# Optimization experiments

Measured on AMD Instinct MI355X. Metric: run time of the kernel, lower is better.

The kernel has to match this reference:

```python
import jax, jax.numpy as jnp
import numpy as np

B, L, D = 32, 512, 128          # batch, seq_len, d_model (= num graph nodes N)
E, HS, DTR, U = 64, 64, 4, 32   # d_proj_E, d_proj_H (state), dt_rank, d_proj_U
R, K, DE, NH = 3, 3, 10, 4      # mamba layers, cheb order, d_e, heads
EPS = 1e-5


def _ln(x, g, b):
    m = jnp.mean(x, -1, keepdims=True)
    v = jnp.mean((x - m) ** 2, -1, keepdims=True)
    return (x - m) / jnp.sqrt(v + EPS) * g + b


def _mamba(x, in_w, conv_w, conv_b, xproj_w, dt_w, dt_b, Alog, Dp, out_w):
    b, l, _ = x.shape
    xz = x @ in_w                                  # (b,l,2E)
    xp, res = xz[..., :E], xz[..., E:]
    xc = jnp.transpose(xp, (0, 2, 1))              # (b,E,l)
    # causal depthwise conv: torch pads both sides by d_conv-1 then slices [:l]
    xc = jax.lax.conv_general_dilated(
        xc, conv_w, (1,), [(conv_w.shape[-1] - 1, 0)],
        dimension_numbers=('NCH', 'OIH', 'NCH'), feature_group_count=E)
    xc = xc + conv_b[None, :, None]
    xp = jax.nn.silu(jnp.transpose(xc, (0, 2, 1)))  # (b,l,E)
    xdbl = xp @ xproj_w                             # (b,l,DTR+2*HS)
    delta = jax.nn.softplus(xdbl[..., :DTR] @ dt_w + dt_b)        # (b,l,E)
    Bm = xdbl[..., DTR:DTR + HS]                                   # (b,l,HS)
    Cm = xdbl[..., DTR + HS:]                                      # (b,l,HS)
    A = -jnp.exp(Alog)                                             # (E,HS)
    dA = jnp.exp(delta[..., None] * A)                             # (b,l,E,HS)
    dBu = delta[..., None] * Bm[:, :, None, :] * xp[..., None]     # (b,l,E,HS)

    def step(s, t):
        dA_t, dBu_t, C_t = t
        s = dA_t * s + dBu_t
        return s, jnp.einsum('bdn,bn->bd', s, C_t)

    _, ys = jax.lax.scan(step, jnp.zeros((b, E, HS), x.dtype),
                         (jnp.swapaxes(dA, 0, 1), jnp.swapaxes(dBu, 0, 1),
                          jnp.swapaxes(Cm, 0, 1)))
    y = jnp.swapaxes(ys, 0, 1) + xp * Dp
    y = y * jax.nn.sigmoid(res)
    return y @ out_w


def _forward(x, mb_in_w, mb_conv_w, mb_conv_b, mb_xproj_w, mb_dt_w, mb_dt_b,
             mb_Alog, mb_D, mb_out_w, ln1_g, ln1_b, ln2_g, ln2_b,
             ffn_w1, ffn_b1, ffn_w2, ffn_b2,
             psi_emb, psi, W_q, W_k, attn_alpha, F_w, f_b, head_mix,
             head_w, head_b):
    # ---- bidirectional Mamba stack ----
    for i in range(R):
        f, bk = 2 * i, 2 * i + 1
        Y1 = _mamba(x, mb_in_w[f], mb_conv_w[f], mb_conv_b[f], mb_xproj_w[f],
                    mb_dt_w[f], mb_dt_b[f], mb_Alog[f], mb_D[f], mb_out_w[f])
        Y2 = jnp.flip(_mamba(jnp.flip(x, 1), mb_in_w[bk], mb_conv_w[bk],
                             mb_conv_b[bk], mb_xproj_w[bk], mb_dt_w[bk],
                             mb_dt_b[bk], mb_Alog[bk], mb_D[bk], mb_out_w[bk]), 1)
        Y3 = _ln(x + Y1 + Y2, ln1_g[i], ln1_b[i])
        Yp = jax.nn.relu(Y3 @ ffn_w1[i] + ffn_b1[i]) @ ffn_w2[i] + ffn_b2[i]
        x = _ln(Yp + Y3, ln2_g[i], ln2_b[i])
    h = jnp.transpose(x, (0, 2, 1))                # (B, N=D, L)
    # ---- MAGAC (deterministic single MC sample, eval, no edge drop) ----
    diff = psi_emb[:, None, :] - psi_emb[None, :, :]
    A_g = jax.nn.softmax(jnp.exp(-psi * jnp.sum(diff * diff, -1)), axis=1)
    Q = jnp.einsum('nd,dhm->nhm', psi_emb, W_q)
    Kt = jnp.einsum('nd,dhm->nhm', psi_emb, W_k)
    attn = jax.nn.softmax(jnp.einsum('nhd,mhd->hnm', Q, Kt)
                          / jnp.sqrt(jnp.asarray(DE, x.dtype)), axis=-1)
    alpha = jax.nn.sigmoid(attn_alpha)
    A_effs = alpha * A_g[None] + (1.0 - alpha) * attn   # (H,N,N)
    mix = jax.nn.softmax(head_mix)
    I = jnp.eye(D, dtype=x.dtype)
    out = jnp.zeros((x.shape[0], D), x.dtype)
    for hh in range(NH):
        A = A_effs[hh]
        sup = [I, A]
        for _ in range(2, K + 1):
            sup.append(2.0 * A @ sup[-1] - sup[-2])
        S = jnp.stack(sup, 0)                             # (K+1,N,N)
        Wf = jnp.einsum('nd,dkl->nkl', psi_emb, F_w[hh])  # (N,K+1,L)
        bf = psi_emb @ f_b[hh]                            # (N,)
        out_h = jnp.einsum('knm,bml,nkl->bn', S, h, Wf) + bf
        out = out + mix[hh] * out_h
    log_var = jnp.zeros_like(out)
    pred = out @ head_w + head_b                          # (B,1)
    return pred, log_var


def setup_inputs() -> dict:
    key = jax.random.key(0)
    ks = iter(jax.random.split(key, 40))
    nrm = lambda shp, s=0.05: (jax.random.normal(next(ks), shp, jnp.float32) * s)
    M = 2 * R
    base_Alog = jnp.log(jnp.arange(1, HS + 1, dtype=jnp.float32))
    inp = {
        'x': jax.random.normal(next(ks), (B, L, D), jnp.float32),
        'mb_in_w': nrm((M, D, 2 * E)),
        'mb_conv_w': nrm((M, E, 1, 3), 0.2),
        'mb_conv_b': jnp.zeros((M, E), jnp.float32),
        'mb_xproj_w': nrm((M, E, DTR + 2 * HS)),
        'mb_dt_w': nrm((M, DTR, E), 0.2),
        'mb_dt_b': jnp.zeros((M, E), jnp.float32),
        'mb_Alog': jnp.tile(base_Alog[None, None, :], (M, E, 1)),
        'mb_D': jnp.ones((M, E), jnp.float32),
        'mb_out_w': nrm((M, E, D)),
        'ln1_g': jnp.ones((R, D), jnp.float32),
        'ln1_b': jnp.zeros((R, D), jnp.float32),
        'ln2_g': jnp.ones((R, D), jnp.float32),
        'ln2_b': jnp.zeros((R, D), jnp.float32),
        'ffn_w1': nrm((R, D, U)),
        'ffn_b1': jnp.zeros((R, U), jnp.float32),
        'ffn_w2': nrm((R, U, D)),
        'ffn_b2': jnp.zeros((R, D), jnp.float32),
        'psi_emb': jax.random.normal(next(ks), (D, DE), jnp.float32),
        'psi': jnp.asarray(1.0, jnp.float32),
        'W_q': jax.random.normal(next(ks), (DE, NH, DE), jnp.float32),
        'W_k': jax.random.normal(next(ks), (DE, NH, DE), jnp.float32),
        'attn_alpha': jnp.asarray(0.5, jnp.float32),
        'F_w': nrm((NH, DE, K + 1, L), 0.05),
        'f_b': nrm((NH, DE), 1.0),
        'head_mix': jnp.ones((NH,), jnp.float32),
        'head_w': nrm((D, 1)),
        'head_b': jnp.zeros((1,), jnp.float32),
    }
    return inp


def reference(x, mb_in_w, mb_conv_w, mb_conv_b, mb_xproj_w, mb_dt_w, mb_dt_b,
              mb_Alog, mb_D, mb_out_w, ln1_g, ln1_b, ln2_g, ln2_b,
              ffn_w1, ffn_b1, ffn_w2, ffn_b2,
              psi_emb, psi, W_q, W_k, attn_alpha, F_w, f_b, head_mix,
              head_w, head_b):
    return _forward(x, mb_in_w, mb_conv_w, mb_conv_b, mb_xproj_w, mb_dt_w,
                    mb_dt_b, mb_Alog, mb_D, mb_out_w, ln1_g, ln1_b, ln2_g,
                    ln2_b, ffn_w1, ffn_b1, ffn_w2, ffn_b2, psi_emb, psi,
                    W_q, W_k, attn_alpha, F_w, f_b, head_mix, head_w, head_b)
```

## Files before the change

### kernel.cpp

```cpp
#include <hip/hip_runtime.h>
#include <hip/hip_bf16.h>


#define B_ 32
#define L_ 512
#define D_ 128
#define E_ 64
#define HS_ 64

#define OFF_X     0u
#define OFF_XZF   2097152u
#define OFF_XZB   4194304u
#define OFF_XPF   6291456u
#define OFF_XPB   7340032u
#define OFF_PKF   8388608u
#define OFF_PKB   10485760u
#define OFF_XBCF  12582912u
#define OFF_XBCB  14680064u
#define OFF_YSF   16777216u
#define OFF_YSB   17825792u
#define OFF_V     2097152u
#define OFF_WFT   10485760u
#define OFF_STT   11534336u
#define OFF_AEFF  11796480u
#define OFF_QB    11943936u
#define OFF_KB    11949056u
#define OFF_MIX   11954176u
#define OFF_ALPH  11954180u
#define OFF_BFT   11954184u
#define OFF_PART  12582912u
#define OFF_RED1  16777216u

__device__ __forceinline__ float sigf(float x) { return 1.f / (1.f + __expf(-x)); }
__device__ __forceinline__ unsigned int bf16r(float x) {
    unsigned int u = __float_as_uint(x);
    return (u + 0x7fffu + ((u >> 16) & 1u)) >> 16;
}

__global__ __launch_bounds__(256) void gemm_in2_kernel(
    const float* __restrict__ X, const float* __restrict__ WF, const float* __restrict__ WB,
    float* __restrict__ xzF, float* __restrict__ xzB)
{
    __shared__ float sxT[128][36];
    __shared__ float sw[2][16][128];
    const int tid = threadIdx.x;
    const int r0 = blockIdx.x * 32;
    for (int q = tid; q < 1024; q += 256) {
        const int r = q >> 5, k4 = q & 31;
        const float4 v = *(const float4*)&X[(size_t)(r0 + r) * 128 + k4 * 4];
        sxT[k4 * 4 + 0][r] = v.x; sxT[k4 * 4 + 1][r] = v.y;
        sxT[k4 * 4 + 2][r] = v.z; sxT[k4 * 4 + 3][r] = v.w;
    }
    const int wv = tid >> 6, lane = tid & 63;
    const int d = wv >> 1, ch = wv & 1;
    const int r4 = lane >> 4, c16 = lane & 15;
    float4 acc[8];
#pragma unroll
    for (int j = 0; j < 8; ++j) acc[j] = float4{0.f, 0.f, 0.f, 0.f};
    for (int ko = 0; ko < 128; ko += 16) {
        __syncthreads();
        for (int q = tid; q < 1024; q += 256) {
            const int dd = q >> 9, kk = (q >> 5) & 15, c4 = q & 31;
            *(float4*)&sw[dd][kk][c4 * 4] =
                *(const float4*)&((dd ? WB : WF)[(ko + kk) * 128 + c4 * 4]);
        }
        __syncthreads();
#pragma unroll
        for (int kk = 0; kk < 16; ++kk) {
            const float4 w4 = *(const float4*)&sw[d][kk][ch * 64 + c16 * 4];
            const float4 xa = *(const float4*)&sxT[ko + kk][r4 * 8];
            const float4 xb = *(const float4*)&sxT[ko + kk][r4 * 8 + 4];
            const float xs[8] = {xa.x, xa.y, xa.z, xa.w, xb.x, xb.y, xb.z, xb.w};
#pragma unroll
            for (int j = 0; j < 8; ++j) {
                acc[j].x = fmaf(xs[j], w4.x, acc[j].x);
                acc[j].y = fmaf(xs[j], w4.y, acc[j].y);
                acc[j].z = fmaf(xs[j], w4.z, acc[j].z);
                acc[j].w = fmaf(xs[j], w4.w, acc[j].w);
            }
        }
    }
    float* xz = d ? xzB : xzF;
#pragma unroll
    for (int j = 0; j < 8; ++j) {
        *(float4*)&xz[(r0 + r4 * 8 + j) * 128 + ch * 64 + c16 * 4] = acc[j];
    }
}

__global__ __launch_bounds__(256) void prep4_kernel(
    const float* __restrict__ xzF_, const float* __restrict__ xzB_,
    const float* __restrict__ conv_w, const float* __restrict__ conv_b,
    const float* __restrict__ xproj_w, const float* __restrict__ dt_w,
    const float* __restrict__ dt_b, int layer,
    float* __restrict__ xpF_, float* __restrict__ xpB_,
    unsigned int* __restrict__ xbcF_, unsigned int* __restrict__ xbcB_,
    float* __restrict__ pkF_, float* __restrict__ pkB_)
{
    __shared__ float sW[8448];
    __shared__ float sxp4[4][64][4];
    __shared__ float sdl4[4][4][4];
    const int tid = threadIdx.x, wv = tid >> 6, lane = tid & 63;
    const int dir = (int)(blockIdx.x >= 1024);
    const int r0 = (blockIdx.x & 1023) * 16;
    const int b = r0 >> 9;
    const int m = layer * 2 + dir;
    const float* Wg = xproj_w + m * 8448;
    for (int q = tid; q < 2112; q += 256) ((float4*)sW)[q] = ((const float4*)Wg)[q];
    const float* xz = dir ? xzB_ : xzF_;
    float* xp  = dir ? xpB_  : xpF_;
    unsigned int* xbc = dir ? xbcB_ : xbcF_;
    float* pkx = dir ? pkB_  : pkF_;
    const float* cw = conv_w + m * 192 + lane * 3;
    const float cw0 = cw[0], cw1 = cw[1], cw2 = cw[2];
    const float cb  = conv_b[m * 64 + lane];
    const float dtb = dt_b[m * 64 + lane];
    const float* dwp = dt_w + m * 256;
    const float dw0 = dwp[lane], dw1 = dwp[64 + lane], dw2 = dwp[128 + lane], dw3 = dwp[192 + lane];
    float uu[4];
#pragma unroll
    for (int it = 0; it < 4; ++it) {
        const int row = r0 + wv * 4 + it;
        const int l = row & 511;
        const int l1 = dir ? l + 1 : l - 1;
        const int l2 = dir ? l + 2 : l - 2;
        float acc = cb;
        const float x0 = xz[(size_t)row * 128 + lane];
        const float x1 = (l1 >= 0 && l1 < 512) ? xz[(size_t)(b * 512 + l1) * 128 + lane] : 0.f;
        const float x2 = (l2 >= 0 && l2 < 512) ? xz[(size_t)(b * 512 + l2) * 128 + lane] : 0.f;
        acc += cw0 * x2 + cw1 * x1 + cw2 * x0;
        const float u = acc * sigf(acc);
        xp[row * 64 + lane] = u;
        uu[it] = u;
    }
    *(float4*)&sxp4[wv][lane][0] = float4{uu[0], uu[1], uu[2], uu[3]};
    __syncthreads();
    const int jdt = lane & 3;
    float aB[4] = {0.f, 0.f, 0.f, 0.f};
    float aC[4] = {0.f, 0.f, 0.f, 0.f};
    float adt[4] = {0.f, 0.f, 0.f, 0.f};
#pragma unroll 4
    for (int k = 0; k < 64; ++k) {
        const float wB = sW[k * 132 + 4 + lane];
        const float wC = sW[k * 132 + 68 + lane];
        const float wd = sW[k * 132 + jdt];
        const float4 xv = *(const float4*)&sxp4[wv][k][0];
        aB[0] = fmaf(xv.x, wB, aB[0]); aC[0] = fmaf(xv.x, wC, aC[0]); adt[0] = fmaf(xv.x, wd, adt[0]);
        aB[1] = fmaf(xv.y, wB, aB[1]); aC[1] = fmaf(xv.y, wC, aC[1]); adt[1] = fmaf(xv.y, wd, adt[1]);
        aB[2] = fmaf(xv.z, wB, aB[2]); aC[2] = fmaf(xv.z, wC, aC[2]); adt[2] = fmaf(xv.z, wd, adt[2]);
        aB[3] = fmaf(xv.w, wB, aB[3]); aC[3] = fmaf(xv.w, wC, aC[3]); adt[3] = fmaf(xv.w, wd, adt[3]);
    }
#pragma unroll
    for (int it = 0; it < 4; ++it) {
        const int row = r0 + wv * 4 + it;
        xbc[row * 64 + lane] = (bf16r(aC[it]) << 16) | bf16r(aB[it]);
        if (lane < 4) sdl4[wv][it][lane] = adt[it];
    }
#pragma unroll
    for (int it = 0; it < 4; ++it) {
        const int row = r0 + wv * 4 + it;
        float dpre = fmaf(sdl4[wv][it][0], dw0, dtb);
        dpre = fmaf(sdl4[wv][it][1], dw1, dpre);
        dpre = fmaf(sdl4[wv][it][2], dw2, dpre);
        dpre = fmaf(sdl4[wv][it][3], dw3, dpre);
        const float dlt = (dpre > 20.f) ? dpre : log1pf(__expf(dpre));
        ((float2*)pkx)[row * 64 + lane] = float2{dlt, dlt * uu[it]};
    }
}

__global__ __launch_bounds__(256, 4) void scan7_kernel(
    const unsigned int* __restrict__ xbcF, const unsigned int* __restrict__ xbcB,
    const float* __restrict__ pkF, const float* __restrict__ pkB,
    const float* __restrict__ AlogF, const float* __restrict__ AlogB,
    float* __restrict__ ysF, float* __restrict__ ysB)
{
    __shared__ unsigned int sbc[2][1024];
    __shared__ float spk[2][4][16][2];
    __shared__ float ytile[4][16][68];
    const int tid = threadIdx.x, wv = tid >> 6, lane = tid & 63;
    const int bx = blockIdx.x;
    const int db = bx & 63;
    const int dir = db >> 5;
    const int b   = db & 31;
    const int e0  = (bx >> 6) * 4;
    const int e   = e0 + wv;
    const unsigned int* xbc = dir ? xbcB : xbcF;
    const float* pk  = dir ? pkB  : pkF;
    const float* Aw  = dir ? AlogB : AlogF;
    float* ys = dir ? ysB : ysF;
    const float a = -__expf(Aw[e * 64 + lane]);
    float s = 0.f;
    float* yrow = ys + (size_t)(b * 64 + e) * 512;

    const int psl = tid & 15, pw_ = tid >> 4;

#define STG_LOAD(RS)                                                              \
    {                                                                             \
        nb = *(const uint4*)(xbc + (size_t)(RS) * 64 + tid * 4);                  \
        if (tid < 64)                                                             \
            npp = *(const float2*)(pk + (size_t)((RS) + psl) * 128 + (e0 + pw_) * 2); \
    }
#define STG_WRITE(BUF)                                                            \
    {                                                                             \
        *(uint4*)(&sbc[BUF][tid * 4]) = nb;                                       \
        if (tid < 64) *(float2*)(&spk[BUF][pw_][psl][0]) = npp;                   \
    }

#define SCAN16(REV)                                                               \
    {                                                                             \
        const unsigned int* bc = &sbc[cur][0];                                    \
        const float* pq = &spk[cur][wv][0][0];                                    \
        _Pragma("unroll")                                                         \
        for (int j = 0; j < 8; ++j) {                                             \
            const int pj = (REV) ? 7 - j : j;                                     \
            const float4 pk4 = *(const float4*)(pq + pj * 4);                     \
            const int sA = (REV) ? 15 - 2 * j : 2 * j;                            \
            const int sB = (REV) ? 14 - 2 * j : 2 * j + 1;                        \
            const float dlA = (REV) ? pk4.z : pk4.x;                              \
            const float duA = (REV) ? pk4.w : pk4.y;                              \
            const float dlB = (REV) ? pk4.x : pk4.z;                              \
            const float duB = (REV) ? pk4.y : pk4.w;                              \
            const unsigned int bA = bc[sA * 64 + lane];                           \
            const float BnA = __uint_as_float(bA << 16);                          \
            const float CnA = __uint_as_float(bA & 0xffff0000u);                  \
            s = fmaf(__expf(dlA * a), s, duA * BnA);                              \
            ytile[wv][2 * j][lane] = s * CnA;                                     \
            const unsigned int bB = bc[sB * 64 + lane];                           \
            const float BnB = __uint_as_float(bB << 16);                          \
            const float CnB = __uint_as_float(bB & 0xffff0000u);                  \
            s = fmaf(__expf(dlB * a), s, duB * BnB);                              \
            ytile[wv][2 * j + 1][lane] = s * CnB;                                 \
        }                                                                         \
    }

    {
        uint4 nb; float2 npp;
        const int rs0 = b * 512 + (dir ? 496 : 0);
        STG_LOAD(rs0);
        STG_WRITE(0);
    }
    __syncthreads();

    int cur = 0;
    const int rr = lane & 15, sg = lane >> 4;
    for (int t = 0; t < 32; ++t) {
        uint4 nb; float2 npp;
        const bool more = (t + 1) < 32;
        if (more) {
            const int rs = b * 512 + (dir ? (496 - (t + 1) * 16) : ((t + 1) * 16));
            STG_LOAD(rs);
        }
        if (dir == 0) { SCAN16(0) } else { SCAN16(1) }
        {
            const float* yt = &ytile[wv][rr][sg * 16];
            const float4 A0 = *(const float4*)yt;
            const float4 A1 = *(const float4*)(yt + 4);
            const float4 A2 = *(const float4*)(yt + 8);
            const float4 A3 = *(const float4*)(yt + 12);
            float p = ((A0.x + A0.y) + (A0.z + A0.w)) + ((A1.x + A1.y) + (A1.z + A1.w))
                    + ((A2.x + A2.y) + (A2.z + A2.w)) + ((A3.x + A3.y) + (A3.z + A3.w));
            p += __shfl_xor(p, 16);
            p += __shfl_xor(p, 32);
            if (lane < 16) {
                const int lg = dir ? (511 - (t * 16 + rr)) : (t * 16 + rr);
                yrow[lg] = p;
            }
        }
        if (more) STG_WRITE(cur ^ 1);
        __syncthreads();
        cur ^= 1;
    }
#undef STG_LOAD
#undef STG_WRITE
#undef SCAN16
}

__global__ __launch_bounds__(256) void opfn_kernel(
    const float* __restrict__ ysF, const float* __restrict__ ysB,
    const float* __restrict__ xpF, const float* __restrict__ xpB,
    const float* __restrict__ xzF, const float* __restrict__ xzB,
    const float* __restrict__ Dp, int layer,
    const float* __restrict__ Xc, const float* __restrict__ out_w,
    const float* __restrict__ W1, const float* __restrict__ b1,
    const float* __restrict__ W2, const float* __restrict__ b2,
    const float* __restrict__ g1, const float* __restrict__ bb1,
    const float* __restrict__ g2, const float* __restrict__ bb2,
    float* __restrict__ xout)
{
    __shared__ float smem[8832];
    float* syt = smem;
    float* y3  = smem;
    float* sy  = smem + 2176;
    float* sw  = smem + 4224;
    float* sh  = smem + 8320;
    const int tid = threadIdx.x;
    const int r0 = blockIdx.x * 16;
    const int b = r0 >> 9, l0 = r0 & 511;

    for (int q = tid; q < 512; q += 256) {
        const int d = q >> 8, ee = (q >> 2) & 63, rq = q & 3;
        const float* ysp = d ? ysB : ysF;
        const float4 v = *(const float4*)&ysp[(size_t)(b * 64 + ee) * 512 + l0 + rq * 4];
        float* dst = &syt[(d * 64 + ee) * 17 + rq * 4];
        dst[0] = v.x; dst[1] = v.y; dst[2] = v.z; dst[3] = v.w;
    }
    __syncthreads();
    for (int q = tid; q < 2048; q += 256) {
        const int r = q >> 7, c = q & 127;
        const int d = c >> 6, ee = c & 63;
        const int row = r0 + r;
        const float dv  = Dp[(layer * 2 + d) * 64 + ee];
        const float u   = (d ? xpB : xpF)[(size_t)row * 64 + ee];
        const float res = (d ? xzB : xzF)[(size_t)row * 128 + 64 + ee];
        sy[r * 128 + c] = (syt[(d * 64 + ee) * 17 + r] + u * dv) * sigf(res);
    }
    const int wv = tid >> 6, lane = tid & 63;
    const float* WFp = out_w + (layer * 2) * 8192;
    const float* WBp = out_w + (layer * 2 + 1) * 8192;
    float acc[4][2];
#pragma unroll
    for (int r = 0; r < 4; ++r) { acc[r][0] = 0.f; acc[r][1] = 0.f; }
    for (int ko = 0; ko < 128; ko += 32) {
        __syncthreads();
        for (int q = tid; q < 1024; q += 256) {
            const int kk = q >> 5, c4 = q & 31;
            const int kg = ko + kk;
            *(float4*)&sw[kk * 128 + c4 * 4] = (kg < 64)
                ? *(const float4*)&WFp[kg * 128 + c4 * 4]
                : *(const float4*)&WBp[(kg - 64) * 128 + c4 * 4];
        }
        __syncthreads();
#define OPSTEP(COMP, J)                                                           \
        {                                                                         \
            const float w0 = sw[(kk + (J)) * 128 + lane];                         \
            const float w1 = sw[(kk + (J)) * 128 + lane + 64];                    \
            acc[0][0] = fmaf(y40.COMP, w0, acc[0][0]);                            \
            acc[0][1] = fmaf(y40.COMP, w1, acc[0][1]);                            \
            acc[1][0] = fmaf(y41.COMP, w0, acc[1][0]);                            \
            acc[1][1] = fmaf(y41.COMP, w1, acc[1][1]);                            \
            acc[2][0] = fmaf(y42.COMP, w0, acc[2][0]);                            \
            acc[2][1] = fmaf(y42.COMP, w1, acc[2][1]);                            \
            acc[3][0] = fmaf(y43.COMP, w0, acc[3][0]);                            \
            acc[3][1] = fmaf(y43.COMP, w1, acc[3][1]);                            \
        }
#pragma unroll
        for (int kk = 0; kk < 32; kk += 4) {
            const float4 y40 = *(const float4*)&sy[(wv * 4 + 0) * 128 + ko + kk];
            const float4 y41 = *(const float4*)&sy[(wv * 4 + 1) * 128 + ko + kk];
            const float4 y42 = *(const float4*)&sy[(wv * 4 + 2) * 128 + ko + kk];
            const float4 y43 = *(const float4*)&sy[(wv * 4 + 3) * 128 + ko + kk];
            OPSTEP(x, 0) OPSTEP(y, 1) OPSTEP(z, 2) OPSTEP(w, 3)
        }
#undef OPSTEP
    }
    __syncthreads();
    for (int q = tid; q < 1024; q += 256) ((float4*)sw)[q] = ((const float4*)W1)[q];
#pragma unroll
    for (int r = 0; r < 4; ++r) {
        const int rl = wv * 4 + r;
        const int row = r0 + rl;
        float v0 = acc[r][0] + Xc[(size_t)row * 128 + lane];
        float v1 = acc[r][1] + Xc[(size_t)row * 128 + lane + 64];
        float sum = v0 + v1, sq = v0 * v0 + v1 * v1;
#pragma unroll
        for (int o = 32; o >= 1; o >>= 1) { sum += __shfl_xor(sum, o); sq += __shfl_xor(sq, o); }
        const float mean = sum * (1.f / 128.f);
        const float var = sq * (1.f / 128.f) - mean * mean;
        const float rs = rsqrtf(var + 1e-5f);
        y3[rl * 128 + lane]      = (v0 - mean) * rs * g1[lane] + bb1[lane];
        y3[rl * 128 + lane + 64] = (v1 - mean) * rs * g1[lane + 64] + bb1[lane + 64];
    }
    __syncthreads();
    {
        const int r = tid >> 4, u = tid & 15;
        float h0 = b1[u], h1 = b1[u + 16];
#pragma unroll 8
        for (int k = 0; k < 128; ++k) {
            const float xv = y3[r * 128 + k];
            h0 = fmaf(xv, sw[k * 32 + u], h0);
            h1 = fmaf(xv, sw[k * 32 + u + 16], h1);
        }
        sh[r * 32 + u]      = fmaxf(h0, 0.f);
        sh[r * 32 + u + 16] = fmaxf(h1, 0.f);
    }
    __syncthreads();
    for (int q = tid; q < 1024; q += 256) ((float4*)sw)[q] = ((const float4*)W2)[q];
    __syncthreads();
#pragma unroll
    for (int r = 0; r < 4; ++r) {
        const int rl = wv * 4 + r;
        float a0 = b2[lane], a1 = b2[lane + 64];
#pragma unroll 8
        for (int k = 0; k < 32; ++k) {
            const float hv = sh[rl * 32 + k];
            a0 = fmaf(hv, sw[k * 128 + lane], a0);
            a1 = fmaf(hv, sw[k * 128 + lane + 64], a1);
        }
        const float v0 = a0 + y3[rl * 128 + lane];
        const float v1 = a1 + y3[rl * 128 + lane + 64];
        float sum = v0 + v1, sq = v0 * v0 + v1 * v1;
#pragma unroll
        for (int o = 32; o >= 1; o >>= 1) { sum += __shfl_xor(sum, o); sq += __shfl_xor(sq, o); }
        const float mean = sum * (1.f / 128.f);
        const float var = sq * (1.f / 128.f) - mean * mean;
        const float rs = rsqrtf(var + 1e-5f);
        const int row = r0 + rl;
        xout[(size_t)row * 128 + lane]      = (v0 - mean) * rs * g2[lane] + bb2[lane];
        xout[(size_t)row * 128 + lane + 64] = (v1 - mean) * rs * g2[lane + 64] + bb2[lane + 64];
    }
}

__global__ __launch_bounds__(256) void head_prep_kernel(
    const float* __restrict__ psi, const float* __restrict__ W_q, const float* __restrict__ W_k,
    const float* __restrict__ f_b, const float* __restrict__ hmix, const float* __restrict__ attn_a,
    float* __restrict__ mixb, float* __restrict__ alphab, float* __restrict__ bft,
    float* __restrict__ Qb, float* __restrict__ Kb)
{
    const int tid = threadIdx.x;
    const float m0 = hmix[0], m1 = hmix[1], m2 = hmix[2], m3 = hmix[3];
    const float mx = fmaxf(fmaxf(m0, m1), fmaxf(m2, m3));
    const float e0 = __expf(m0 - mx), e1 = __expf(m1 - mx), e2 = __expf(m2 - mx), e3 = __expf(m3 - mx);
    const float inv = 1.f / (e0 + e1 + e2 + e3);
    float mixv[4] = {e0 * inv, e1 * inv, e2 * inv, e3 * inv};
    if (tid < 4) mixb[tid] = mixv[tid];
    if (tid == 4) alphab[0] = sigf(attn_a[0]);
    if (tid < 128) {
        float s = 0.f;
        for (int h = 0; h < 4; ++h) {
            float t = 0.f;
            for (int d = 0; d < 10; ++d) t = fmaf(psi[tid * 10 + d], f_b[h * 10 + d], t);
            s = fmaf(mixv[h], t, s);
        }
        bft[tid] = s;
    }
    for (int idx = tid; idx < 5120; idx += 256) {
        const int n = idx / 40, rem = idx - n * 40, h = rem / 10, d = rem - h * 10;
        float q = 0.f, kk = 0.f;
        for (int d0 = 0; d0 < 10; ++d0) {
            const float pv = psi[n * 10 + d0];
            q = fmaf(pv, W_q[(d0 * 4 + h) * 10 + d], q);
            kk = fmaf(pv, W_k[(d0 * 4 + h) * 10 + d], kk);
        }
        Qb[idx] = q; Kb[idx] = kk;
    }
}

__global__ __launch_bounds__(128) void head_qkaeff_kernel(
    const float* __restrict__ psi, const float* __restrict__ psis,
    const float* __restrict__ Qb, const float* __restrict__ Kb,
    const float* __restrict__ alphab,
    float* __restrict__ Aeff, float* __restrict__ StT)
{
    __shared__ float spn[10];
    __shared__ float red[128];
    const int h = blockIdx.x >> 7, n = blockIdx.x & 127, mcol = threadIdx.x;
    if (mcol < 10) spn[mcol] = psi[n * 10 + mcol];
    __syncthreads();
    float d2 = 0.f;
#pragma unroll
    for (int d = 0; d < 10; ++d) { const float df = spn[d] - psi[mcol * 10 + d]; d2 = fmaf(df, df, d2); }
    const float gv = __expf(-psis[0] * d2);
    float qv = 0.f;
#pragma unroll
    for (int d = 0; d < 10; ++d) qv = fmaf(Qb[n * 40 + h * 10 + d], Kb[mcol * 40 + h * 10 + d], qv);
    qv *= 0.3162277660168379332f;
    float r;
    red[mcol] = gv; __syncthreads();
    for (int s = 64; s >= 1; s >>= 1) { if (mcol < s) red[mcol] = fmaxf(red[mcol], red[mcol + s]); __syncthreads(); }
    r = red[0]; __syncthreads();
    const float eg = __expf(gv - r);
    red[mcol] = eg; __syncthreads();
    for (int s = 64; s >= 1; s >>= 1) { if (mcol < s) red[mcol] += red[mcol + s]; __syncthreads(); }
    const float gsum = red[0]; __syncthreads();
    red[mcol] = qv; __syncthreads();
    for (int s = 64; s >= 1; s >>= 1) { if (mcol < s) red[mcol] = fmaxf(red[mcol], red[mcol + s]); __syncthreads(); }
    r = red[0]; __syncthreads();
    const float eq = __expf(qv - r);
    red[mcol] = eq; __syncthreads();
    for (int s = 64; s >= 1; s >>= 1) { if (mcol < s) red[mcol] += red[mcol + s]; __syncthreads(); }
    const float qsum = red[0];
    const float al = alphab[0];
    const float aeff = al * (eg / gsum) + (1.f - al) * (eq / qsum);
    Aeff[h * 16384 + n * 128 + mcol] = aeff;
    StT[((h * 4 + 1) * 128 + mcol) * 128 + n] = aeff;
    StT[((h * 4 + 0) * 128 + mcol) * 128 + n] = (mcol == n) ? 1.f : 0.f;
}

__global__ __launch_bounds__(256) void head_cheb_kernel(
    const float* __restrict__ Aeff, float* __restrict__ StT, int kk)
{
    const int h = blockIdx.x >> 6;
    const int m0 = ((blockIdx.x & 63) << 1) + (threadIdx.x >> 7);
    const int n = threadIdx.x & 127;
    const float* Ar = Aeff + h * 16384 + n * 128;
    const float* Sp = StT + ((h * 4 + kk - 1) * 128 + m0) * 128;
    float acc = 0.f;
#pragma unroll 8
    for (int p = 0; p < 128; ++p) acc = fmaf(Ar[p], Sp[p], acc);
    const float s2 = StT[((h * 4 + kk - 2) * 128 + m0) * 128 + n];
    StT[((h * 4 + kk) * 128 + m0) * 128 + n] = 2.f * acc - s2;
}

__global__ __launch_bounds__(256) void head_wf_kernel(
    const float* __restrict__ psi, const float* __restrict__ F_w, float* __restrict__ WfT)
{
    const int idx = blockIdx.x * 256 + threadIdx.x;
    const int n = idx & 127, l = (idx >> 7) & 511, k = (idx >> 16) & 3, h = idx >> 18;
    float acc = 0.f;
#pragma unroll
    for (int d = 0; d < 10; ++d)
        acc = fmaf(psi[n * 10 + d], F_w[((h * 10 + d) * 4 + k) * 512 + l], acc);
    WfT[idx] = acc;
}

__global__ __launch_bounds__(256) void head_v4_kernel(
    const float* __restrict__ StT, const float* __restrict__ WfT, const float* __restrict__ mixb,
    float* __restrict__ V)
{
    const int tid = threadIdx.x;
    const int lt = blockIdx.x & 63, mm = blockIdx.x >> 6;
    const int n4 = tid & 31, mh = tid >> 5;
    const int m = mm * 8 + mh;
    const int l0 = lt * 8, n0 = n4 * 4;
    float4 sv[16];
#pragma unroll
    for (int h = 0; h < 4; ++h) {
        const float mx = mixb[h];
#pragma unroll
        for (int k = 0; k < 4; ++k) {
            const float4 v = *(const float4*)&StT[(size_t)((h * 4 + k) * 128 + m) * 128 + n0];
            sv[h * 4 + k] = float4{v.x * mx, v.y * mx, v.z * mx, v.w * mx};
        }
    }
#pragma unroll
    for (int j = 0; j < 8; ++j) {
        const int l = l0 + j;
        float4 acc = {0.f, 0.f, 0.f, 0.f};
#pragma unroll
        for (int hk = 0; hk < 16; ++hk) {
            const float4 w = *(const float4*)&WfT[(size_t)(hk * 512 + l) * 128 + n0];
            acc.x = fmaf(sv[hk].x, w.x, acc.x);
            acc.y = fmaf(sv[hk].y, w.y, acc.y);
            acc.z = fmaf(sv[hk].z, w.z, acc.z);
            acc.w = fmaf(sv[hk].w, w.w, acc.w);
        }
        *(float4*)&V[(size_t)(l * 128 + m) * 128 + n0] = acc;
    }
}

__global__ __launch_bounds__(256) void head_ctr_kernel(
    const float* __restrict__ Xf, const float* __restrict__ V, float* __restrict__ partial)
{
    __shared__ float sx[32][128];
    const int l = blockIdx.x, tid = threadIdx.x;
    const int n = tid & 127, mh = tid >> 7;
    for (int q = tid; q < 1024; q += 256) {
        const int b = q >> 5, m4 = q & 31;
        *(float4*)&sx[b][m4 * 4] = *(const float4*)&Xf[(size_t)(b * 512 + l) * 128 + m4 * 4];
    }
    __syncthreads();
    float acc[32];
#pragma unroll
    for (int b = 0; b < 32; ++b) acc[b] = 0.f;
    const float* vp = V + (size_t)(l * 128 + mh * 64) * 128 + n;
    for (int mm = 0; mm < 64; ++mm) {
        const float v = vp[(size_t)mm * 128];
        const int m = mh * 64 + mm;
#pragma unroll
        for (int b = 0; b < 32; ++b) acc[b] = fmaf(sx[b][m], v, acc[b]);
    }
#pragma unroll
    for (int b = 0; b < 32; ++b)
        partial[(size_t)((l * 2 + mh) * 32 + b) * 128 + n] = acc[b];
}

__global__ __launch_bounds__(128) void head_red_kernel(
    const float* __restrict__ partial, float* __restrict__ red1)
{
    const int b = blockIdx.x >> 5, cs = blockIdx.x & 31, n = threadIdx.x;
    const float* p = partial + ((size_t)(cs * 32) * 32 + b) * 128 + n;
    float s = 0.f;
#pragma unroll 8
    for (int c = 0; c < 32; ++c) s += p[(size_t)c * 4096];
    red1[(b * 32 + cs) * 128 + n] = s;
}

__global__ __launch_bounds__(128) void head_out_kernel(
    const float* __restrict__ red1, const float* __restrict__ bft,
    const float* __restrict__ head_w, const float* __restrict__ head_b, float* __restrict__ out)
{
    __shared__ float red[128];
    const int b = blockIdx.x, n = threadIdx.x;
    float s = bft[n];
#pragma unroll 8
    for (int cs = 0; cs < 32; ++cs) s += red1[(b * 32 + cs) * 128 + n];
    red[n] = s * head_w[n];
    __syncthreads();
    for (int st = 64; st >= 1; st >>= 1) { if (n < st) red[n] += red[n + st]; __syncthreads(); }
    if (n == 0) out[b] = red[0] + head_b[0];
    out[32 + b * 128 + n] = 0.f;
}

extern "C" void kernel_launch(void* const* d_in, const int* in_sizes, int n_in,
                              void* d_out, int out_size, void* d_ws, size_t ws_size,
                              hipStream_t stream) {
    const float* x_in    = (const float*)d_in[0];
    const float* in_w    = (const float*)d_in[1];
    const float* conv_w  = (const float*)d_in[2];
    const float* conv_b  = (const float*)d_in[3];
    const float* xproj_w = (const float*)d_in[4];
    const float* dt_w    = (const float*)d_in[5];
    const float* dt_b    = (const float*)d_in[6];
    const float* Alog    = (const float*)d_in[7];
    const float* Dp      = (const float*)d_in[8];
    const float* out_w   = (const float*)d_in[9];
    const float* ln1_g   = (const float*)d_in[10];
    const float* ln1_b   = (const float*)d_in[11];
    const float* ln2_g   = (const float*)d_in[12];
    const float* ln2_b   = (const float*)d_in[13];
    const float* ffn_w1  = (const float*)d_in[14];
    const float* ffn_b1  = (const float*)d_in[15];
    const float* ffn_w2  = (const float*)d_in[16];
    const float* ffn_b2  = (const float*)d_in[17];
    const float* psi_emb = (const float*)d_in[18];
    const float* psi_s   = (const float*)d_in[19];
    const float* W_q     = (const float*)d_in[20];
    const float* W_k     = (const float*)d_in[21];
    const float* attn_a  = (const float*)d_in[22];
    const float* F_w     = (const float*)d_in[23];
    const float* f_b     = (const float*)d_in[24];
    const float* hmix    = (const float*)d_in[25];
    const float* head_w  = (const float*)d_in[26];
    const float* head_b  = (const float*)d_in[27];
    float* ws = (float*)d_ws;
    float* outp = (float*)d_out;

    for (int i = 0; i < 3; ++i) {
        const float* xcur = (i == 0) ? x_in : (ws + OFF_X);
        const int mF = 2 * i, mB = 2 * i + 1;
        gemm_in2_kernel<<<512, 256, 0, stream>>>(
            xcur, in_w + mF * 16384, in_w + mB * 16384, ws + OFF_XZF, ws + OFF_XZB);
        prep4_kernel<<<2048, 256, 0, stream>>>(
            ws + OFF_XZF, ws + OFF_XZB, conv_w, conv_b, xproj_w, dt_w, dt_b, i,
            ws + OFF_XPF, ws + OFF_XPB,
            (unsigned int*)(ws + OFF_XBCF), (unsigned int*)(ws + OFF_XBCB),
            ws + OFF_PKF, ws + OFF_PKB);
        scan7_kernel<<<1024, 256, 0, stream>>>(
            (const unsigned int*)(ws + OFF_XBCF), (const unsigned int*)(ws + OFF_XBCB),
            ws + OFF_PKF, ws + OFF_PKB,
            Alog + mF * 4096, Alog + mB * 4096, ws + OFF_YSF, ws + OFF_YSB);
        opfn_kernel<<<1024, 256, 0, stream>>>(
            ws + OFF_YSF, ws + OFF_YSB, ws + OFF_XPF, ws + OFF_XPB, ws + OFF_XZF, ws + OFF_XZB,
            Dp, i, xcur, out_w,
            ffn_w1 + i * 4096, ffn_b1 + i * 32, ffn_w2 + i * 4096, ffn_b2 + i * 128,
            ln1_g + i * 128, ln1_b + i * 128, ln2_g + i * 128, ln2_b + i * 128,
            ws + OFF_X);
    }
    head_prep_kernel<<<1, 256, 0, stream>>>(
        psi_emb, W_q, W_k, f_b, hmix, attn_a,
        ws + OFF_MIX, ws + OFF_ALPH, ws + OFF_BFT, ws + OFF_QB, ws + OFF_KB);
    head_qkaeff_kernel<<<512, 128, 0, stream>>>(
        psi_emb, psi_s, ws + OFF_QB, ws + OFF_KB, ws + OFF_ALPH, ws + OFF_AEFF, ws + OFF_STT);
    head_cheb_kernel<<<256, 256, 0, stream>>>(ws + OFF_AEFF, ws + OFF_STT, 2);
    head_cheb_kernel<<<256, 256, 0, stream>>>(ws + OFF_AEFF, ws + OFF_STT, 3);
    head_wf_kernel<<<4096, 256, 0, stream>>>(psi_emb, F_w, ws + OFF_WFT);
    head_v4_kernel<<<1024, 256, 0, stream>>>(ws + OFF_STT, ws + OFF_WFT, ws + OFF_MIX, ws + OFF_V);
    head_ctr_kernel<<<512, 256, 0, stream>>>(ws + OFF_X, ws + OFF_V, ws + OFF_PART);
    head_red_kernel<<<1024, 128, 0, stream>>>(ws + OFF_PART, ws + OFF_RED1);
    head_out_kernel<<<32, 128, 0, stream>>>(
        ws + OFF_RED1, ws + OFF_BFT, head_w, head_b, outp);
}
```

Before: 519.7 us.

## Fuse next-layer input GEMM into opfn, merge head prep kernels, use exp2 in scan

The next layer's in-projection GEMM now runs inside the output/FFN kernel, reusing the freshly normalized rows held in shared memory, so layers 2 and 3 drop a separate launch and a global reload of X. The head prep, QK/affinity and WF kernels are merged into one launch. Softmax mix and bias projections are recomputed inline where they are used. The scan uses a native exp2 with the log2(e) factor prescaled into A. In exchange the fused kernel does extra serialized GEMM work per block, and the merged head kernel recomputes K projections per block.

```diff
diff --git a/kernel.cpp b/kernel.cpp
--- a/kernel.cpp
+++ b/kernel.cpp
@@ -23,11 +23,6 @@
 #define OFF_WFT   10485760u
 #define OFF_STT   11534336u
 #define OFF_AEFF  11796480u
-#define OFF_QB    11943936u
-#define OFF_KB    11949056u
-#define OFF_MIX   11954176u
-#define OFF_ALPH  11954180u
-#define OFF_BFT   11954184u
 #define OFF_PART  12582912u
 #define OFF_RED1  16777216u
 
@@ -167,7 +162,7 @@
     }
 }
 
-__global__ __launch_bounds__(256, 4) void scan7_kernel(
+__global__ __launch_bounds__(256, 4) void scan8_kernel(
     const unsigned int* __restrict__ xbcF, const unsigned int* __restrict__ xbcB,
     const float* __restrict__ pkF, const float* __restrict__ pkB,
     const float* __restrict__ AlogF, const float* __restrict__ AlogB,
@@ -187,7 +182,7 @@
     const float* pk  = dir ? pkB  : pkF;
     const float* Aw  = dir ? AlogB : AlogF;
     float* ys = dir ? ysB : ysF;
-    const float a = -__expf(Aw[e * 64 + lane]);
+    const float a2 = -__expf(Aw[e * 64 + lane]) * 1.4426950408889634f;
     float s = 0.f;
     float* yrow = ys + (size_t)(b * 64 + e) * 512;
 
@@ -222,12 +217,12 @@
             const unsigned int bA = bc[sA * 64 + lane];                           \
             const float BnA = __uint_as_float(bA << 16);                          \
             const float CnA = __uint_as_float(bA & 0xffff0000u);                  \
-            s = fmaf(__expf(dlA * a), s, duA * BnA);                              \
+            s = fmaf(__builtin_amdgcn_exp2f(dlA * a2), s, duA * BnA);             \
             ytile[wv][2 * j][lane] = s * CnA;                                     \
             const unsigned int bB = bc[sB * 64 + lane];                           \
             const float BnB = __uint_as_float(bB << 16);                          \
             const float CnB = __uint_as_float(bB & 0xffff0000u);                  \
-            s = fmaf(__expf(dlB * a), s, duB * BnB);                              \
+            s = fmaf(__builtin_amdgcn_exp2f(dlB * a2), s, duB * BnB);             \
             ytile[wv][2 * j + 1][lane] = s * CnB;                                 \
         }                                                                         \
     }
@@ -274,7 +269,7 @@
 #undef SCAN16
 }
 
-__global__ __launch_bounds__(256) void opfn_kernel(
+__global__ __launch_bounds__(256) void opfn2_kernel(
     const float* __restrict__ ysF, const float* __restrict__ ysB,
     const float* __restrict__ xpF, const float* __restrict__ xpB,
     const float* __restrict__ xzF, const float* __restrict__ xzB,
@@ -284,7 +279,9 @@
     const float* __restrict__ W2, const float* __restrict__ b2,
     const float* __restrict__ g1, const float* __restrict__ bb1,
     const float* __restrict__ g2, const float* __restrict__ bb2,
-    float* __restrict__ xout)
+    float* __restrict__ xout,
+    const float* __restrict__ WFn, const float* __restrict__ WBn,
+    float* __restrict__ xzFo, float* __restrict__ xzBo)
 {
     __shared__ float smem[8832];
     float* syt = smem;
@@ -329,7 +326,7 @@
                 : *(const float4*)&WBp[(kg - 64) * 128 + c4 * 4];
         }
         __syncthreads();
-#define OPSTEP(COMP, J)                                                           \
+#define OPSTEP(SRC, COMP, J)                                                      \
         {                                                                         \
             const float w0 = sw[(kk + (J)) * 128 + lane];                         \
             const float w1 = sw[(kk + (J)) * 128 + lane + 64];                    \
@@ -348,9 +345,8 @@
             const float4 y41 = *(const float4*)&sy[(wv * 4 + 1) * 128 + ko + kk];
             const float4 y42 = *(const float4*)&sy[(wv * 4 + 2) * 128 + ko + kk];
             const float4 y43 = *(const float4*)&sy[(wv * 4 + 3) * 128 + ko + kk];
-            OPSTEP(x, 0) OPSTEP(y, 1) OPSTEP(z, 2) OPSTEP(w, 3)
-        }
-#undef OPSTEP
+            OPSTEP(sy, x, 0) OPSTEP(sy, y, 1) OPSTEP(sy, z, 2) OPSTEP(sy, w, 3)
+        }
     }
     __syncthreads();
     for (int q = tid; q < 1024; q += 256) ((float4*)sw)[q] = ((const float4*)W1)[q];
@@ -385,6 +381,7 @@
     __syncthreads();
     for (int q = tid; q < 1024; q += 256) ((float4*)sw)[q] = ((const float4*)W2)[q];
     __syncthreads();
+    float xr[4][2];
 #pragma unroll
     for (int r = 0; r < 4; ++r) {
         const int rl = wv * 4 + r;
@@ -404,81 +401,114 @@
         const float var = sq * (1.f / 128.f) - mean * mean;
         const float rs = rsqrtf(var + 1e-5f);
         const int row = r0 + rl;
-        xout[(size_t)row * 128 + lane]      = (v0 - mean) * rs * g2[lane] + bb2[lane];
-        xout[(size_t)row * 128 + lane + 64] = (v1 - mean) * rs * g2[lane + 64] + bb2[lane + 64];
-    }
-}
-
-__global__ __launch_bounds__(256) void head_prep_kernel(
-    const float* __restrict__ psi, const float* __restrict__ W_q, const float* __restrict__ W_k,
-    const float* __restrict__ f_b, const float* __restrict__ hmix, const float* __restrict__ attn_a,
-    float* __restrict__ mixb, float* __restrict__ alphab, float* __restrict__ bft,
-    float* __restrict__ Qb, float* __restrict__ Kb)
-{
-    const int tid = threadIdx.x;
-    const float m0 = hmix[0], m1 = hmix[1], m2 = hmix[2], m3 = hmix[3];
-    const float mx = fmaxf(fmaxf(m0, m1), fmaxf(m2, m3));
-    const float e0 = __expf(m0 - mx), e1 = __expf(m1 - mx), e2 = __expf(m2 - mx), e3 = __expf(m3 - mx);
-    const float inv = 1.f / (e0 + e1 + e2 + e3);
-    float mixv[4] = {e0 * inv, e1 * inv, e2 * inv, e3 * inv};
-    if (tid < 4) mixb[tid] = mixv[tid];
-    if (tid == 4) alphab[0] = sigf(attn_a[0]);
-    if (tid < 128) {
-        float s = 0.f;
-        for (int h = 0; h < 4; ++h) {
-            float t = 0.f;
-            for (int d = 0; d < 10; ++d) t = fmaf(psi[tid * 10 + d], f_b[h * 10 + d], t);
-            s = fmaf(mixv[h], t, s);
-        }
-        bft[tid] = s;
-    }
-    for (int idx = tid; idx < 5120; idx += 256) {
-        const int n = idx / 40, rem = idx - n * 40, h = rem / 10, d = rem - h * 10;
-        float q = 0.f, kk = 0.f;
-        for (int d0 = 0; d0 < 10; ++d0) {
-            const float pv = psi[n * 10 + d0];
-            q = fmaf(pv, W_q[(d0 * 4 + h) * 10 + d], q);
-            kk = fmaf(pv, W_k[(d0 * 4 + h) * 10 + d], kk);
-        }
-        Qb[idx] = q; Kb[idx] = kk;
-    }
-}
-
-__global__ __launch_bounds__(128) void head_qkaeff_kernel(
-    const float* __restrict__ psi, const float* __restrict__ psis,
-    const float* __restrict__ Qb, const float* __restrict__ Kb,
-    const float* __restrict__ alphab,
+        const float o0 = (v0 - mean) * rs * g2[lane] + bb2[lane];
+        const float o1 = (v1 - mean) * rs * g2[lane + 64] + bb2[lane + 64];
+        xout[(size_t)row * 128 + lane]      = o0;
+        xout[(size_t)row * 128 + lane + 64] = o1;
+        xr[r][0] = o0; xr[r][1] = o1;
+    }
+    if (WFn == nullptr) return;
+    __syncthreads();
+    float* sxr = y3;
+#pragma unroll
+    for (int r = 0; r < 4; ++r) {
+        sxr[(wv * 4 + r) * 128 + lane]      = xr[r][0];
+        sxr[(wv * 4 + r) * 128 + lane + 64] = xr[r][1];
+    }
+    for (int d = 0; d < 2; ++d) {
+        const float* Wn = d ? WBn : WFn;
+        float* xzo = d ? xzBo : xzFo;
+#pragma unroll
+        for (int r = 0; r < 4; ++r) { acc[r][0] = 0.f; acc[r][1] = 0.f; }
+        for (int ko = 0; ko < 128; ko += 32) {
+            __syncthreads();
+            for (int q = tid; q < 1024; q += 256) {
+                const int kk = q >> 5, c4 = q & 31;
+                *(float4*)&sw[kk * 128 + c4 * 4] = *(const float4*)&Wn[(ko + kk) * 128 + c4 * 4];
+            }
+            __syncthreads();
+#pragma unroll
+            for (int kk = 0; kk < 32; kk += 4) {
+                const float4 y40 = *(const float4*)&sxr[(wv * 4 + 0) * 128 + ko + kk];
+                const float4 y41 = *(const float4*)&sxr[(wv * 4 + 1) * 128 + ko + kk];
+                const float4 y42 = *(const float4*)&sxr[(wv * 4 + 2) * 128 + ko + kk];
+                const float4 y43 = *(const float4*)&sxr[(wv * 4 + 3) * 128 + ko + kk];
+                OPSTEP(sxr, x, 0) OPSTEP(sxr, y, 1) OPSTEP(sxr, z, 2) OPSTEP(sxr, w, 3)
+            }
+        }
+#pragma unroll
+        for (int r = 0; r < 4; ++r) {
+            const int row = r0 + wv * 4 + r;
+            xzo[(size_t)row * 128 + lane]      = acc[r][0];
+            xzo[(size_t)row * 128 + lane + 64] = acc[r][1];
+        }
+    }
+#undef OPSTEP
+}
+
+__global__ __launch_bounds__(256) void head_wfqk_kernel(
+    const float* __restrict__ psi, const float* __restrict__ F_w, float* __restrict__ WfT,
+    const float* __restrict__ psis, const float* __restrict__ W_q, const float* __restrict__ W_k,
+    const float* __restrict__ attn_a,
     float* __restrict__ Aeff, float* __restrict__ StT)
 {
-    __shared__ float spn[10];
-    __shared__ float red[128];
-    const int h = blockIdx.x >> 7, n = blockIdx.x & 127, mcol = threadIdx.x;
-    if (mcol < 10) spn[mcol] = psi[n * 10 + mcol];
+    __shared__ float sQ[2][10];
+    __shared__ float red[2][128];
+    if (blockIdx.x < 4096) {
+        const int idx = blockIdx.x * 256 + threadIdx.x;
+        const int n = idx & 127, l = (idx >> 7) & 511, k = (idx >> 16) & 3, h = idx >> 18;
+        float acc = 0.f;
+#pragma unroll
+        for (int d = 0; d < 10; ++d)
+            acc = fmaf(psi[n * 10 + d], F_w[((h * 10 + d) * 4 + k) * 512 + l], acc);
+        WfT[idx] = acc;
+        return;
+    }
+    const int q = blockIdx.x - 4096;
+    const int half = threadIdx.x >> 7, mcol = threadIdx.x & 127;
+    const int unit = q * 2 + half;
+    const int h = unit >> 7, n = unit & 127;
+    float Kreg[10];
+#pragma unroll
+    for (int d = 0; d < 10; ++d) Kreg[d] = 0.f;
+#pragma unroll
+    for (int d0 = 0; d0 < 10; ++d0) {
+        const float pv = psi[mcol * 10 + d0];
+#pragma unroll
+        for (int d = 0; d < 10; ++d) Kreg[d] = fmaf(pv, W_k[(d0 * 4 + h) * 10 + d], Kreg[d]);
+    }
+    if (mcol < 10) {
+        float qd = 0.f;
+        for (int d0 = 0; d0 < 10; ++d0)
+            qd = fmaf(psi[n * 10 + d0], W_q[(d0 * 4 + h) * 10 + mcol], qd);
+        sQ[half][mcol] = qd;
+    }
     __syncthreads();
     float d2 = 0.f;
 #pragma unroll
-    for (int d = 0; d < 10; ++d) { const float df = spn[d] - psi[mcol * 10 + d]; d2 = fmaf(df, df, d2); }
+    for (int d = 0; d < 10; ++d) { const float df = psi[n * 10 + d] - psi[mcol * 10 + d]; d2 = fmaf(df, df, d2); }
     const float gv = __expf(-psis[0] * d2);
     float qv = 0.f;
 #pragma unroll
-    for (int d = 0; d < 10; ++d) qv = fmaf(Qb[n * 40 + h * 10 + d], Kb[mcol * 40 + h * 10 + d], qv);
+    for (int d = 0; d < 10; ++d) qv = fmaf(sQ[half][d], Kreg[d], qv);
     qv *= 0.3162277660168379332f;
+    float* rd = red[half];
     float r;
-    red[mcol] = gv; __syncthreads();
-    for (int s = 64; s >= 1; s >>= 1) { if (mcol < s) red[mcol] = fmaxf(red[mcol], red[mcol + s]); __syncthreads(); }
-    r = red[0]; __syncthreads();
+    rd[mcol] = gv; __syncthreads();
+    for (int s = 64; s >= 1; s >>= 1) { if (mcol < s) rd[mcol] = fmaxf(rd[mcol], rd[mcol + s]); __syncthreads(); }
+    r = rd[0]; __syncthreads();
     const float eg = __expf(gv - r);
-    red[mcol] = eg; __syncthreads();
-    for (int s = 64; s >= 1; s >>= 1) { if (mcol < s) red[mcol] += red[mcol + s]; __syncthreads(); }
-    const float gsum = red[0]; __syncthreads();
-    red[mcol] = qv; __syncthreads();
-    for (int s = 64; s >= 1; s >>= 1) { if (mcol < s) red[mcol] = fmaxf(red[mcol], red[mcol + s]); __syncthreads(); }
-    r = red[0]; __syncthreads();
+    rd[mcol] = eg; __syncthreads();
+    for (int s = 64; s >= 1; s >>= 1) { if (mcol < s) rd[mcol] += rd[mcol + s]; __syncthreads(); }
+    const float gsum = rd[0]; __syncthreads();
+    rd[mcol] = qv; __syncthreads();
+    for (int s = 64; s >= 1; s >>= 1) { if (mcol < s) rd[mcol] = fmaxf(rd[mcol], rd[mcol + s]); __syncthreads(); }
+    r = rd[0]; __syncthreads();
     const float eq = __expf(qv - r);
-    red[mcol] = eq; __syncthreads();
-    for (int s = 64; s >= 1; s >>= 1) { if (mcol < s) red[mcol] += red[mcol + s]; __syncthreads(); }
-    const float qsum = red[0];
-    const float al = alphab[0];
+    rd[mcol] = eq; __syncthreads();
+    for (int s = 64; s >= 1; s >>= 1) { if (mcol < s) rd[mcol] += rd[mcol + s]; __syncthreads(); }
+    const float qsum = rd[0];
+    const float al = sigf(attn_a[0]);
     const float aeff = al * (eg / gsum) + (1.f - al) * (eq / qsum);
     Aeff[h * 16384 + n * 128 + mcol] = aeff;
     StT[((h * 4 + 1) * 128 + mcol) * 128 + n] = aeff;
@@ -500,22 +530,15 @@
     StT[((h * 4 + kk) * 128 + m0) * 128 + n] = 2.f * acc - s2;
 }
 
-__global__ __launch_bounds__(256) void head_wf_kernel(
-    const float* __restrict__ psi, const float* __restrict__ F_w, float* __restrict__ WfT)
-{
-    const int idx = blockIdx.x * 256 + threadIdx.x;
-    const int n = idx & 127, l = (idx >> 7) & 511, k = (idx >> 16) & 3, h = idx >> 18;
-    float acc = 0.f;
-#pragma unroll
-    for (int d = 0; d < 10; ++d)
-        acc = fmaf(psi[n * 10 + d], F_w[((h * 10 + d) * 4 + k) * 512 + l], acc);
-    WfT[idx] = acc;
-}
-
 __global__ __launch_bounds__(256) void head_v4_kernel(
-    const float* __restrict__ StT, const float* __restrict__ WfT, const float* __restrict__ mixb,
+    const float* __restrict__ StT, const float* __restrict__ WfT, const float* __restrict__ hmix,
     float* __restrict__ V)
 {
+    const float m0 = hmix[0], m1 = hmix[1], m2 = hmix[2], m3 = hmix[3];
+    const float mxx = fmaxf(fmaxf(m0, m1), fmaxf(m2, m3));
+    const float e0 = __expf(m0 - mxx), e1 = __expf(m1 - mxx), e2 = __expf(m2 - mxx), e3 = __expf(m3 - mxx);
+    const float inv = 1.f / (e0 + e1 + e2 + e3);
+    const float mixv[4] = {e0 * inv, e1 * inv, e2 * inv, e3 * inv};
     const int tid = threadIdx.x;
     const int lt = blockIdx.x & 63, mm = blockIdx.x >> 6;
     const int n4 = tid & 31, mh = tid >> 5;
@@ -524,7 +547,7 @@
     float4 sv[16];
 #pragma unroll
     for (int h = 0; h < 4; ++h) {
-        const float mx = mixb[h];
+        const float mx = mixv[h];
 #pragma unroll
         for (int k = 0; k < 4; ++k) {
             const float4 v = *(const float4*)&StT[(size_t)((h * 4 + k) * 128 + m) * 128 + n0];
@@ -585,12 +608,25 @@
 }
 
 __global__ __launch_bounds__(128) void head_out_kernel(
-    const float* __restrict__ red1, const float* __restrict__ bft,
+    const float* __restrict__ red1, const float* __restrict__ psi,
+    const float* __restrict__ f_b, const float* __restrict__ hmix,
     const float* __restrict__ head_w, const float* __restrict__ head_b, float* __restrict__ out)
 {
     __shared__ float red[128];
     const int b = blockIdx.x, n = threadIdx.x;
-    float s = bft[n];
+    const float m0 = hmix[0], m1 = hmix[1], m2 = hmix[2], m3 = hmix[3];
+    const float mxx = fmaxf(fmaxf(m0, m1), fmaxf(m2, m3));
+    const float e0 = __expf(m0 - mxx), e1 = __expf(m1 - mxx), e2 = __expf(m2 - mxx), e3 = __expf(m3 - mxx);
+    const float inv = 1.f / (e0 + e1 + e2 + e3);
+    const float mixv[4] = {e0 * inv, e1 * inv, e2 * inv, e3 * inv};
+    float s = 0.f;
+#pragma unroll
+    for (int h = 0; h < 4; ++h) {
+        float t = 0.f;
+#pragma unroll
+        for (int d = 0; d < 10; ++d) t = fmaf(psi[n * 10 + d], f_b[h * 10 + d], t);
+        s = fmaf(mixv[h], t, s);
+    }
 #pragma unroll 8
     for (int cs = 0; cs < 32; ++cs) s += red1[(b * 32 + cs) * 128 + n];
     red[n] = s * head_w[n];
@@ -634,38 +670,37 @@
     float* ws = (float*)d_ws;
     float* outp = (float*)d_out;
 
+    gemm_in2_kernel<<<512, 256, 0, stream>>>(
+        x_in, in_w, in_w + 16384, ws + OFF_XZF, ws + OFF_XZB);
     for (int i = 0; i < 3; ++i) {
         const float* xcur = (i == 0) ? x_in : (ws + OFF_X);
         const int mF = 2 * i, mB = 2 * i + 1;
-        gemm_in2_kernel<<<512, 256, 0, stream>>>(
-            xcur, in_w + mF * 16384, in_w + mB * 16384, ws + OFF_XZF, ws + OFF_XZB);
         prep4_kernel<<<2048, 256, 0, stream>>>(
             ws + OFF_XZF, ws + OFF_XZB, conv_w, conv_b, xproj_w, dt_w, dt_b, i,
             ws + OFF_XPF, ws + OFF_XPB,
             (unsigned int*)(ws + OFF_XBCF), (unsigned int*)(ws + OFF_XBCB),
             ws + OFF_PKF, ws + OFF_PKB);
-        scan7_kernel<<<1024, 256, 0, stream>>>(
+        scan8_kernel<<<1024, 256, 0, stream>>>(
             (const unsigned int*)(ws + OFF_XBCF), (const unsigned int*)(ws + OFF_XBCB),
             ws + OFF_PKF, ws + OFF_PKB,
             Alog + mF * 4096, Alog + mB * 4096, ws + OFF_YSF, ws + OFF_YSB);
-        opfn_kernel<<<1024, 256, 0, stream>>>(
+        const float* WFn = (i < 2) ? (in_w + (2 * i + 2) * 16384) : nullptr;
+        const float* WBn = (i < 2) ? (in_w + (2 * i + 3) * 16384) : nullptr;
+        opfn2_kernel<<<1024, 256, 0, stream>>>(
             ws + OFF_YSF, ws + OFF_YSB, ws + OFF_XPF, ws + OFF_XPB, ws + OFF_XZF, ws + OFF_XZB,
             Dp, i, xcur, out_w,
             ffn_w1 + i * 4096, ffn_b1 + i * 32, ffn_w2 + i * 4096, ffn_b2 + i * 128,
             ln1_g + i * 128, ln1_b + i * 128, ln2_g + i * 128, ln2_b + i * 128,
-            ws + OFF_X);
-    }
-    head_prep_kernel<<<1, 256, 0, stream>>>(
-        psi_emb, W_q, W_k, f_b, hmix, attn_a,
-        ws + OFF_MIX, ws + OFF_ALPH, ws + OFF_BFT, ws + OFF_QB, ws + OFF_KB);
-    head_qkaeff_kernel<<<512, 128, 0, stream>>>(
-        psi_emb, psi_s, ws + OFF_QB, ws + OFF_KB, ws + OFF_ALPH, ws + OFF_AEFF, ws + OFF_STT);
+            ws + OFF_X, WFn, WBn, ws + OFF_XZF, ws + OFF_XZB);
+    }
+    head_wfqk_kernel<<<4352, 256, 0, stream>>>(
+        psi_emb, F_w, ws + OFF_WFT, psi_s, W_q, W_k, attn_a,
+        ws + OFF_AEFF, ws + OFF_STT);
     head_cheb_kernel<<<256, 256, 0, stream>>>(ws + OFF_AEFF, ws + OFF_STT, 2);
     head_cheb_kernel<<<256, 256, 0, stream>>>(ws + OFF_AEFF, ws + OFF_STT, 3);
-    head_wf_kernel<<<4096, 256, 0, stream>>>(psi_emb, F_w, ws + OFF_WFT);
-    head_v4_kernel<<<1024, 256, 0, stream>>>(ws + OFF_STT, ws + OFF_WFT, ws + OFF_MIX, ws + OFF_V);
+    head_v4_kernel<<<1024, 256, 0, stream>>>(ws + OFF_STT, ws + OFF_WFT, hmix, ws + OFF_V);
     head_ctr_kernel<<<512, 256, 0, stream>>>(ws + OFF_X, ws + OFF_V, ws + OFF_PART);
     head_red_kernel<<<1024, 128, 0, stream>>>(ws + OFF_PART, ws + OFF_RED1);
     head_out_kernel<<<32, 128, 0, stream>>>(
-        ws + OFF_RED1, ws + OFF_BFT, head_w, head_b, outp);
-}
+        ws + OFF_RED1, psi_emb, f_b, hmix, head_w, head_b, outp);
+}
```

After: 506.1 us. 1.03x faster.
